# Optimization experiments

Hardware: AMD Instinct MI355X
Metric: run time of the kernel (lower is better)

The kernel has to match this reference:

```python
import jax, jax.numpy as jnp
import numpy as np

HEADS = 8
QK_DIM = 128
V_DIM = 128
QTD = 128   # query_token_dim
TTD = 128   # tgt_token_dim
B = 16384
H, W = 8, 6


def setup_inputs() -> dict:
    key = jax.random.key(0)
    ks = jax.random.split(key, 10)

    def lin(k, out_d, in_d):
        return jax.random.normal(k, (out_d, in_d), jnp.float32) * 0.02

    return {
        "query": jax.random.normal(ks[0], (1, 8, QTD), jnp.float32),
        "tgt_token": jax.random.normal(ks[1], (B, H * W, TTD), jnp.float32),
        "g1": jnp.ones((QTD,), jnp.float32),
        "b1": jnp.zeros((QTD,), jnp.float32),
        "Wq": lin(ks[2], QK_DIM, QTD), "bq": jnp.zeros((QK_DIM,), jnp.float32),
        "Wk": lin(ks[3], QK_DIM, TTD), "bk": jnp.zeros((QK_DIM,), jnp.float32),
        "Wv": lin(ks[4], V_DIM, TTD), "bv": jnp.zeros((V_DIM,), jnp.float32),
        "Wp": lin(ks[5], QTD, V_DIM), "bp": jnp.zeros((QTD,), jnp.float32),
        "g2": jnp.ones((QTD,), jnp.float32),
        "b2": jnp.zeros((QTD,), jnp.float32),
        "Wf1": lin(ks[6], QTD, QTD), "bf1": jnp.zeros((QTD,), jnp.float32),
        "Wf2": lin(ks[7], QTD, QTD), "bf2": jnp.zeros((QTD,), jnp.float32),
        "size_h": H,
        "size_w": W,
    }


def _ln(x, g, b, eps=1e-5):
    m = jnp.mean(x, axis=-1, keepdims=True)
    v = jnp.var(x, axis=-1, keepdims=True)
    return (x - m) * jax.lax.rsqrt(v + eps) * g + b


def _broad_mha(q, k, v):
    # BroadMultiHeadAttention: q [nq, Cq] broadcast over batch; k [Bk,M,Cq]; v [Bk,M,Cv]
    nq, Cq = q.shape
    Bk, M, Cv = v.shape
    d = Cq // HEADS
    qh = q.reshape(nq, HEADS, d).transpose(1, 0, 2)                   # [h, nq, d]
    kh = k.reshape(Bk, M, HEADS, d).transpose(0, 2, 1, 3)             # [b, h, M, d]
    vh = v.reshape(Bk, M, HEADS, Cv // HEADS).transpose(0, 2, 1, 3)   # [b, h, M, dv]
    dots = jnp.einsum('hid,bhjd->bhij', qh, kh) * (d ** -0.5)
    attn = jax.nn.softmax(dots, axis=-1)
    out = jnp.einsum('bhij,bhjd->bhid', attn, vh)                     # [b, h, nq, dv]
    return out.transpose(0, 2, 1, 3).reshape(Bk, nq, Cv)


def _forward(query, tgt_token, g1, b1, Wq, bq, Wk, bk, Wv, bv, Wp, bp,
             g2, b2, Wf1, bf1, Wf2, bf2, Hh, Ww):
    short_cut = query
    qn = _ln(query, g1, b1)
    q = qn @ Wq.T + bq            # [1, 8, qk_dim]
    k = tgt_token @ Wk.T + bk     # [B, HW, qk_dim]
    v = tgt_token @ Wv.T + bv     # [B, HW, v_dim]
    Bk = k.shape[0]
    q0 = q[0]                     # [8, qk_dim] (Q.squeeze() in the original)
    res = [_broad_mha(q0[:2], k, v)]
    k4 = k.reshape(Bk, Hh, Ww, QK_DIM)
    v4 = v.reshape(Bk, Hh, Ww, V_DIM)
    hs = [(0, Hh // 2), (Hh // 2, Hh)]
    ws = [(0, Ww // 3), (Ww // 3, 2 * (Ww // 3)), (2 * (Ww // 3), Ww)]
    idx = 0
    for h0, h1 in hs:
        for w0, w1 in ws:
            kw = k4[:, h0:h1, w0:w1].reshape(Bk, -1, QK_DIM)
            vw = v4[:, h0:h1, w0:w1].reshape(Bk, -1, V_DIM)
            res.append(_broad_mha(q0[2 + idx:3 + idx], kw, vw))
            idx += 1
    x = jnp.concatenate(res, axis=1)   # [B, 8, v_dim]
    x = short_cut + (x @ Wp.T + bp)    # broadcast residual: [1,8,D] + [B,8,D]
    y = _ln(x, g2, b2)
    y = jax.nn.gelu(y @ Wf1.T + bf1, approximate=False) @ Wf2.T + bf2
    return x + y


def reference(query, tgt_token, g1, b1, Wq, bq, Wk, bk, Wv, bv, Wp, bp,
              g2, b2, Wf1, bf1, Wf2, bf2, size_h, size_w):
    return _forward(query, tgt_token, g1, b1, Wq, bq, Wk, bk, Wv, bv, Wp, bp,
                    g2, b2, Wf1, bf1, Wf2, bf2, int(size_h), int(size_w))
```

## Files before the change

kernel.cpp:

```cpp
#include <hip/hip_runtime.h>
#include <math.h>


typedef __bf16 v8bf __attribute__((ext_vector_type(8)));
typedef float  v4f  __attribute__((ext_vector_type(4)));

static __device__ __forceinline__ v4f mfma16(v8bf a, v8bf b, v4f c) {
  return __builtin_amdgcn_mfma_f32_16x16x32_bf16(a, b, c, 0, 0, 0);
}

static __device__ __forceinline__ v8bf cvt8(const float* __restrict__ p) {
  float4 a = *(const float4*)p;
  float4 b = *(const float4*)(p + 4);
  v8bf f;
  f[0] = (__bf16)a.x; f[1] = (__bf16)a.y; f[2] = (__bf16)a.z; f[3] = (__bf16)a.w;
  f[4] = (__bf16)b.x; f[5] = (__bf16)b.y; f[6] = (__bf16)b.z; f[7] = (__bf16)b.w;
  return f;
}

__global__ __launch_bounds__(256)
void prep_kernel(const float* __restrict__ query,
                 const float* __restrict__ g1, const float* __restrict__ b1,
                 const float* __restrict__ Wq, const float* __restrict__ bq,
                 const float* __restrict__ Wk, const float* __restrict__ bk,
                 __bf16* __restrict__ qw, float* __restrict__ qb)
{
  __shared__ float qn[8*128];
  __shared__ float qp[8*128];
  const int t = threadIdx.x;
  for (int idx = t; idx < 1024; idx += 256) qn[idx] = query[idx];
  __syncthreads();
  {
    const int w = t >> 6, L = t & 63;
    const int row = 2*w + (L >> 5), col = L & 31;
    float x[4], s = 0.f, sq = 0.f;
    for (int p = 0; p < 4; p++) { x[p] = qn[row*128 + col + 32*p]; s += x[p]; sq += x[p]*x[p]; }
    for (int m = 1; m < 32; m <<= 1) { s += __shfl_xor(s, m); sq += __shfl_xor(sq, m); }
    const float mean = s * (1.f/128.f);
    const float var  = sq * (1.f/128.f) - mean*mean;
    const float rs   = rsqrtf(var + 1e-5f);
    for (int p = 0; p < 4; p++) {
      const int e = col + 32*p;
      qn[row*128 + e] = (x[p]-mean)*rs*g1[e] + b1[e];
    }
  }
  __syncthreads();
  {
    const int i = t >> 5, o0 = t & 31;
    for (int p = 0; p < 4; p++) {
      const int o = o0 + 32*p;
      float acc = bq[o];
      for (int e = 0; e < 128; e++) acc += qn[i*128 + e] * Wq[o*128 + e];
      qp[i*128 + o] = acc;
    }
  }
  __syncthreads();
  {
    const int cc = t >> 2, e0 = (t & 3) * 32;
    const int h = cc >> 3, i = cc & 7;
    float qv[16];
    for (int d = 0; d < 16; d++) qv[d] = qp[i*128 + 16*h + d];
    for (int e = e0; e < e0 + 32; e++) {
      float acc = 0.f;
      for (int d = 0; d < 16; d++) acc += qv[d] * Wk[(16*h + d)*128 + e];
      qw[cc*136 + e] = (__bf16)(0.25f * acc);
    }
    if (t < 64) {
      const int h2 = t >> 3, i2 = t & 7;
      float acc = 0.f;
      for (int d = 0; d < 16; d++) acc += qp[i2*128 + 16*h2 + d] * bk[16*h2 + d];
      qb[t] = 0.25f * acc;
    }
  }
}

__global__ __launch_bounds__(256)
void conv_kernel(const float* __restrict__ Wv, const float* __restrict__ Wp,
                 const float* __restrict__ Wf1, const float* __restrict__ Wf2,
                 __bf16* __restrict__ dst)
{
  const int m = blockIdx.x;
  const float* src = (m == 0) ? Wv : (m == 1) ? Wp : (m == 2) ? Wf1 : Wf2;
  __bf16* d = dst + m*16384;
  for (int i = threadIdx.x; i < 2048; i += 256)
    *(v8bf*)&d[i*8] = cvt8(&src[i*8]);
}

__global__ __launch_bounds__(256, 4)
void attn_kernel(const float* __restrict__ tgt,
                 const float* __restrict__ bv,
                 const __bf16* __restrict__ qw,
                 const float* __restrict__ qb,
                 const __bf16* __restrict__ wv,
                 float* __restrict__ xout)
{
  __shared__ __align__(16) __bf16 s_tgt[48*136];
  __shared__ __align__(16) __bf16 s_P[64*72];
  __shared__ __align__(16) __bf16 s_vT[128*72];

  const int b  = blockIdx.x;
  const int t  = threadIdx.x;
  const int w  = t >> 6;
  const int L  = t & 63;
  const int ln = L & 15;
  const int g  = L >> 4;

  for (int p = 0; p < 8; p++) {
    const int idx = 64*p + L;
    s_vT[(w*32 + (idx >> 4))*72 + 48 + (idx & 15)] = (__bf16)0.f;
  }
  for (int p = 0; p < 4; p++) {
    const int idx = 64*p + L;
    s_P[(w*16 + (idx >> 4))*72 + 48 + (idx & 15)] = (__bf16)0.f;
  }

  {
    const float* tg = tgt + (long)b * 6144;
    for (int c8 = t; c8 < 768; c8 += 256) {
      v8bf v = cvt8(&tg[c8*8]);
      *(v8bf*)&s_tgt[(c8 >> 4)*136 + (c8 & 15)*8] = v;
    }
  }
  __syncthreads();

  const int c = w*16 + ln;

  v4f dacc[3], vacc[3][2];
  {
    v8bf qwf[4], wvf[2][4];
    for (int ks = 0; ks < 4; ks++)
      qwf[ks] = *(const v8bf*)&qw[c*136 + ks*32 + g*8];
    for (int nt = 0; nt < 2; nt++)
      for (int ks = 0; ks < 4; ks++)
        wvf[nt][ks] = *(const v8bf*)&wv[(w*32 + nt*16 + ln)*128 + ks*32 + g*8];
    const v4f z = {0.f, 0.f, 0.f, 0.f};
    for (int mt = 0; mt < 3; mt++) { dacc[mt] = z; vacc[mt][0] = z; vacc[mt][1] = z; }
    for (int mt = 0; mt < 3; mt++) {
      v8bf af[4];
      for (int ks = 0; ks < 4; ks++)
        af[ks] = *(const v8bf*)&s_tgt[(mt*16 + ln)*136 + ks*32 + g*8];
      for (int ks = 0; ks < 4; ks++) {
        dacc[mt]    = mfma16(af[ks], qwf[ks],    dacc[mt]);
        vacc[mt][0] = mfma16(af[ks], wvf[0][ks], vacc[mt][0]);
        vacc[mt][1] = mfma16(af[ks], wvf[1][ks], vacc[mt][1]);
      }
    }
  }

  {
    const int i = c & 7;
    const float qbv = qb[c];
    const bool allv = (i < 2);
    int hsp = 0, wsp = 0;
    if (!allv) { const int idx = i - 2; hsp = idx / 3; wsp = idx - 3*hsp; }
    float dv[12];
    float mx = -1e30f;
    for (int mt = 0; mt < 3; mt++)
      for (int r = 0; r < 4; r++) {
        const int j  = mt*16 + g*4 + r;
        const int rr = j / 6, ccol = j - rr*6;
        const bool valid = allv || (((rr >> 2) == hsp) && ((ccol >> 1) == wsp));
        const float dd = valid ? dacc[mt][r] + qbv : -1e30f;
        dv[mt*4 + r] = dd;
        mx = fmaxf(mx, dd);
      }
    mx = fmaxf(mx, __shfl_xor(mx, 16));
    mx = fmaxf(mx, __shfl_xor(mx, 32));
    float sm = 0.f;
    for (int p = 0; p < 12; p++) {
      const float e = (dv[p] > -1e29f) ? __expf(dv[p] - mx) : 0.f;
      dv[p] = e; sm += e;
    }
    sm += __shfl_xor(sm, 16);
    sm += __shfl_xor(sm, 32);
    const float inv = 1.f / sm;
    for (int mt = 0; mt < 3; mt++)
      for (int r = 0; r < 4; r++)
        s_P[c*72 + mt*16 + g*4 + r] = (__bf16)(dv[mt*4 + r] * inv);
    for (int nt = 0; nt < 2; nt++) {
      const int o = w*32 + nt*16 + ln;
      const float bvo = bv[o];
      for (int mt = 0; mt < 3; mt++)
        for (int r = 0; r < 4; r++)
          s_vT[o*72 + mt*16 + g*4 + r] = (__bf16)(vacc[mt][nt][r] + bvo);
    }
  }

  {
    const v4f z = {0.f,0.f,0.f,0.f};
    v4f oacc[2] = {z, z};
    for (int ks = 0; ks < 2; ks++) {
      v8bf pf = *(const v8bf*)&s_P[(w*16 + ln)*72 + ks*32 + g*8];
      for (int nt = 0; nt < 2; nt++) {
        v8bf vf = *(const v8bf*)&s_vT[(w*32 + nt*16 + ln)*72 + ks*32 + g*8];
        oacc[nt] = mfma16(pf, vf, oacc[nt]);
      }
    }
    const int ntv = g >> 1;
    const int o = w*32 + ntv*16 + ln;
    float* xo = xout + (long)b * 1024;
    for (int r = 0; r < 4; r++) {
      const int i = (g*4 + r) & 7;
      xo[i*128 + o] = oacc[ntv][r];
    }
  }
}

__global__ __launch_bounds__(256, 4)
void mlp_kernel(const float* __restrict__ query,
                const float* __restrict__ bp,
                const float* __restrict__ g2, const float* __restrict__ b2,
                const float* __restrict__ bf1, const float* __restrict__ bf2,
                const __bf16* __restrict__ wp,
                const __bf16* __restrict__ wf1,
                const __bf16* __restrict__ wf2,
                float* __restrict__ xio)
{
  __shared__ __align__(16) __bf16 s_xn[4][16*136];
  __shared__ __align__(16) __bf16 s_h [4][16*136];

  const int t  = threadIdx.x;
  const int w  = t >> 6, L = t & 63;
  const int ln = L & 15, g = L >> 4;
  const long row0 = (long)blockIdx.x*64 + w*16;
  float* base = xio + row0*128;

  v8bf af[4];
  for (int ks = 0; ks < 4; ks++)
    af[ks] = cvt8(&base[ln*128 + ks*32 + g*8]);

  float x[8][4];
  for (int nt = 0; nt < 8; nt++) {
    v4f acc = {0.f, 0.f, 0.f, 0.f};
    for (int ks = 0; ks < 4; ks++) {
      v8bf wf = *(const v8bf*)&wp[(nt*16 + ln)*128 + ks*32 + g*8];
      acc = mfma16(af[ks], wf, acc);
    }
    const int col = nt*16 + ln;
    const float bpv = bp[col];
    for (int r = 0; r < 4; r++)
      x[nt][r] = acc[r] + bpv + query[((4*g + r) & 7)*128 + col];
  }

  float rmean[4], rrs[4];
  for (int r = 0; r < 4; r++) {
    float s = 0.f, sq = 0.f;
    for (int nt = 0; nt < 8; nt++) { s += x[nt][r]; sq += x[nt][r]*x[nt][r]; }
    for (int m = 1; m < 16; m <<= 1) { s += __shfl_xor(s, m); sq += __shfl_xor(sq, m); }
    const float mean = s * (1.f/128.f);
    const float var  = sq * (1.f/128.f) - mean*mean;
    rmean[r] = mean;
    rrs[r]   = rsqrtf(var + 1e-5f);
  }
  for (int nt = 0; nt < 8; nt++) {
    const int col = nt*16 + ln;
    const float gv = g2[col], b2v = b2[col];
    for (int r = 0; r < 4; r++)
      s_xn[w][(4*g + r)*136 + col] = (__bf16)((x[nt][r] - rmean[r])*rrs[r]*gv + b2v);
  }
  v8bf xf[4];
  for (int ks = 0; ks < 4; ks++)
    xf[ks] = *(const v8bf*)&s_xn[w][ln*136 + ks*32 + g*8];

  for (int nt = 0; nt < 8; nt++) {
    v4f acc = {0.f, 0.f, 0.f, 0.f};
    for (int ks = 0; ks < 4; ks++) {
      v8bf wf = *(const v8bf*)&wf1[(nt*16 + ln)*128 + ks*32 + g*8];
      acc = mfma16(xf[ks], wf, acc);
    }
    const int col = nt*16 + ln;
    const float b1v = bf1[col];
    for (int r = 0; r < 4; r++) {
      const float xx = acc[r] + b1v;
      s_h[w][(4*g + r)*136 + col] = (__bf16)(0.5f*xx*(1.f + erff(xx*0.70710678118654752f)));
    }
  }
  v8bf hf[4];
  for (int ks = 0; ks < 4; ks++)
    hf[ks] = *(const v8bf*)&s_h[w][ln*136 + ks*32 + g*8];

  for (int nt = 0; nt < 8; nt++) {
    v4f acc = {0.f, 0.f, 0.f, 0.f};
    for (int ks = 0; ks < 4; ks++) {
      v8bf wf = *(const v8bf*)&wf2[(nt*16 + ln)*128 + ks*32 + g*8];
      acc = mfma16(hf[ks], wf, acc);
    }
    const int col = nt*16 + ln;
    const float b2v = bf2[col];
    for (int r = 0; r < 4; r++)
      base[(4*g + r)*128 + col] = x[nt][r] + acc[r] + b2v;
  }
}

extern "C" void kernel_launch(void* const* d_in, const int* in_sizes, int n_in,
                              void* d_out, int out_size, void* d_ws, size_t ws_size,
                              hipStream_t stream)
{
  const float* query = (const float*)d_in[0];
  const float* tgt   = (const float*)d_in[1];
  const float* g1    = (const float*)d_in[2];
  const float* b1    = (const float*)d_in[3];
  const float* Wq    = (const float*)d_in[4];
  const float* bq    = (const float*)d_in[5];
  const float* Wk    = (const float*)d_in[6];
  const float* bk    = (const float*)d_in[7];
  const float* Wv    = (const float*)d_in[8];
  const float* bv    = (const float*)d_in[9];
  const float* Wp    = (const float*)d_in[10];
  const float* bp    = (const float*)d_in[11];
  const float* g2    = (const float*)d_in[12];
  const float* b2    = (const float*)d_in[13];
  const float* Wf1   = (const float*)d_in[14];
  const float* bf1   = (const float*)d_in[15];
  const float* Wf2   = (const float*)d_in[16];
  const float* bf2   = (const float*)d_in[17];
  float* out = (float*)d_out;

  __bf16* qw  = (__bf16*)d_ws;
  float*  qb  = (float*)((char*)d_ws + 64*136*2);
  __bf16* wbf = (__bf16*)((char*)d_ws + 64*136*2 + 256);

  const int nB = in_sizes[1] / (48 * 128);

  prep_kernel<<<1, 256, 0, stream>>>(query, g1, b1, Wq, bq, Wk, bk, qw, qb);
  conv_kernel<<<4, 256, 0, stream>>>(Wv, Wp, Wf1, Wf2, wbf);
  attn_kernel<<<nB, 256, 0, stream>>>(tgt, bv, qw, qb, wbf , out);
  mlp_kernel<<<nB/8, 256, 0, stream>>>(query, bp, g2, b2, bf1, bf2,
                                       wbf + 16384, wbf + 2*16384, wbf + 3*16384,
                                       out);
}
```

Before: 775.4 us.

## Fuse attention and MLP into one kernel with prefetched double-buffered tokens

Replaces the separate attention and MLP kernels with one kernel where each block handles 8 batch items. It keeps the attention output in shared memory as bf16 instead of writing it to global memory and reading it back. The next item's target tokens are prefetched into registers and staged through a double-buffered shared tile, and the two weight-prep kernels are merged into one launch. The cost is about 71 KB of shared memory per block and 8 serial iterations per block, which lowers occupancy and the number of blocks that can run at once.

```diff
diff --git a/kernel.cpp b/kernel.cpp
--- a/kernel.cpp
+++ b/kernel.cpp
@@ -18,16 +18,34 @@
   return f;
 }
 
+static __device__ __forceinline__ v8bf cvt2x4(float4 a, float4 b) {
+  v8bf f;
+  f[0] = (__bf16)a.x; f[1] = (__bf16)a.y; f[2] = (__bf16)a.z; f[3] = (__bf16)a.w;
+  f[4] = (__bf16)b.x; f[5] = (__bf16)b.y; f[6] = (__bf16)b.z; f[7] = (__bf16)b.w;
+  return f;
+}
+
 __global__ __launch_bounds__(256)
-void prep_kernel(const float* __restrict__ query,
-                 const float* __restrict__ g1, const float* __restrict__ b1,
-                 const float* __restrict__ Wq, const float* __restrict__ bq,
-                 const float* __restrict__ Wk, const float* __restrict__ bk,
-                 __bf16* __restrict__ qw, float* __restrict__ qb)
+void prep_conv_kernel(const float* __restrict__ query,
+                      const float* __restrict__ g1, const float* __restrict__ b1,
+                      const float* __restrict__ Wq, const float* __restrict__ bq,
+                      const float* __restrict__ Wk, const float* __restrict__ bk,
+                      const float* __restrict__ Wv, const float* __restrict__ Wp,
+                      const float* __restrict__ Wf1, const float* __restrict__ Wf2,
+                      __bf16* __restrict__ qw, float* __restrict__ qb,
+                      __bf16* __restrict__ wdst)
 {
   __shared__ float qn[8*128];
   __shared__ float qp[8*128];
   const int t = threadIdx.x;
+  const int m = blockIdx.x;
+  if (m < 4) {
+    const float* src = (m == 0) ? Wv : (m == 1) ? Wp : (m == 2) ? Wf1 : Wf2;
+    __bf16* d = wdst + m*16384;
+    for (int i = t; i < 2048; i += 256)
+      *(v8bf*)&d[i*8] = cvt8(&src[i*8]);
+    return;
+  }
   for (int idx = t; idx < 1024; idx += 256) qn[idx] = query[idx];
   __syncthreads();
   {
@@ -35,7 +53,7 @@
     const int row = 2*w + (L >> 5), col = L & 31;
     float x[4], s = 0.f, sq = 0.f;
     for (int p = 0; p < 4; p++) { x[p] = qn[row*128 + col + 32*p]; s += x[p]; sq += x[p]*x[p]; }
-    for (int m = 1; m < 32; m <<= 1) { s += __shfl_xor(s, m); sq += __shfl_xor(sq, m); }
+    for (int mm = 1; mm < 32; mm <<= 1) { s += __shfl_xor(s, mm); sq += __shfl_xor(sq, mm); }
     const float mean = s * (1.f/128.f);
     const float var  = sq * (1.f/128.f) - mean*mean;
     const float rs   = rsqrtf(var + 1e-5f);
@@ -74,36 +92,35 @@
   }
 }
 
-__global__ __launch_bounds__(256)
-void conv_kernel(const float* __restrict__ Wv, const float* __restrict__ Wp,
-                 const float* __restrict__ Wf1, const float* __restrict__ Wf2,
-                 __bf16* __restrict__ dst)
+__global__ __launch_bounds__(256, 4)
+void fused2_kernel(const float* __restrict__ tgt,
+                   const float* __restrict__ query,
+                   const float* __restrict__ qb,
+                   const float* __restrict__ bv,
+                   const float* __restrict__ bp,
+                   const float* __restrict__ g2, const float* __restrict__ b2,
+                   const float* __restrict__ bf1, const float* __restrict__ bf2,
+                   const __bf16* __restrict__ qw,
+                   const __bf16* __restrict__ wv,
+                   const __bf16* __restrict__ wp,
+                   const __bf16* __restrict__ wf1,
+                   const __bf16* __restrict__ wf2,
+                   float* __restrict__ out)
 {
-  const int m = blockIdx.x;
-  const float* src = (m == 0) ? Wv : (m == 1) ? Wp : (m == 2) ? Wf1 : Wf2;
-  __bf16* d = dst + m*16384;
-  for (int i = threadIdx.x; i < 2048; i += 256)
-    *(v8bf*)&d[i*8] = cvt8(&src[i*8]);
-}
-
-__global__ __launch_bounds__(256, 4)
-void attn_kernel(const float* __restrict__ tgt,
-                 const float* __restrict__ bv,
-                 const __bf16* __restrict__ qw,
-                 const float* __restrict__ qb,
-                 const __bf16* __restrict__ wv,
-                 float* __restrict__ xout)
-{
-  __shared__ __align__(16) __bf16 s_tgt[48*136];
-  __shared__ __align__(16) __bf16 s_P[64*72];
-  __shared__ __align__(16) __bf16 s_vT[128*72];
-
-  const int b  = blockIdx.x;
+  __shared__ __align__(16) char smem[71168];
+  __bf16* const s_tgt0 = (__bf16*)smem;
+  __bf16* const s_P    = (__bf16*)(smem + 26112);
+  __bf16* const s_vT   = (__bf16*)(smem + 35328);
+  __bf16* const s_act  = (__bf16*)(smem + 53760);
+  __bf16* const s_h    = (__bf16*)smem;
+  __bf16* const s_xn   = (__bf16*)(smem + 35328);
+
   const int t  = threadIdx.x;
   const int w  = t >> 6;
   const int L  = t & 63;
   const int ln = L & 15;
   const int g  = L >> 4;
+  const long b0 = (long)blockIdx.x * 8;
 
   for (int p = 0; p < 8; p++) {
     const int idx = 64*p + L;
@@ -114,120 +131,123 @@
     s_P[(w*16 + (idx >> 4))*72 + 48 + (idx & 15)] = (__bf16)0.f;
   }
 
+  const int c = w*16 + ln;
+  const float qbv = qb[c];
+  const int qi = c & 7;
+  const bool allv = (qi < 2);
+  int hsp = 0, wsp = 0;
+  if (!allv) { const int idx = qi - 2; hsp = idx / 3; wsp = idx - 3*hsp; }
+
+  float4 pf[6];
   {
-    const float* tg = tgt + (long)b * 6144;
-    for (int c8 = t; c8 < 768; c8 += 256) {
-      v8bf v = cvt8(&tg[c8*8]);
-      *(v8bf*)&s_tgt[(c8 >> 4)*136 + (c8 & 15)*8] = v;
-    }
-  }
-  __syncthreads();
-
-  const int c = w*16 + ln;
-
-  v4f dacc[3], vacc[3][2];
-  {
-    v8bf qwf[4], wvf[2][4];
-    for (int ks = 0; ks < 4; ks++)
-      qwf[ks] = *(const v8bf*)&qw[c*136 + ks*32 + g*8];
-    for (int nt = 0; nt < 2; nt++)
+    const float* tg = tgt + b0 * 6144;
+#pragma unroll
+    for (int k2 = 0; k2 < 3; k2++) {
+      pf[2*k2]   = *(const float4*)&tg[(t + k2*256)*8];
+      pf[2*k2+1] = *(const float4*)&tg[(t + k2*256)*8 + 4];
+    }
+  }
+
+  for (int bi = 0; bi < 8; bi++) {
+    __bf16* const s_tgt = s_tgt0 + (bi & 1) * 6528;
+
+#pragma unroll
+    for (int k2 = 0; k2 < 3; k2++) {
+      const int c8 = t + k2*256;
+      *(v8bf*)&s_tgt[(c8 >> 4)*136 + (c8 & 15)*8] = cvt2x4(pf[2*k2], pf[2*k2+1]);
+    }
+    __syncthreads();
+
+    if (bi < 7) {
+      const float* tg = tgt + (b0 + bi + 1) * 6144;
+#pragma unroll
+      for (int k2 = 0; k2 < 3; k2++) {
+        pf[2*k2]   = *(const float4*)&tg[(t + k2*256)*8];
+        pf[2*k2+1] = *(const float4*)&tg[(t + k2*256)*8 + 4];
+      }
+    }
+
+    v4f dacc[3], vacc[3][2];
+    {
+      v8bf qwf[4], wvf[2][4];
       for (int ks = 0; ks < 4; ks++)
-        wvf[nt][ks] = *(const v8bf*)&wv[(w*32 + nt*16 + ln)*128 + ks*32 + g*8];
-    const v4f z = {0.f, 0.f, 0.f, 0.f};
-    for (int mt = 0; mt < 3; mt++) { dacc[mt] = z; vacc[mt][0] = z; vacc[mt][1] = z; }
-    for (int mt = 0; mt < 3; mt++) {
-      v8bf af[4];
-      for (int ks = 0; ks < 4; ks++)
-        af[ks] = *(const v8bf*)&s_tgt[(mt*16 + ln)*136 + ks*32 + g*8];
-      for (int ks = 0; ks < 4; ks++) {
-        dacc[mt]    = mfma16(af[ks], qwf[ks],    dacc[mt]);
-        vacc[mt][0] = mfma16(af[ks], wvf[0][ks], vacc[mt][0]);
-        vacc[mt][1] = mfma16(af[ks], wvf[1][ks], vacc[mt][1]);
-      }
-    }
-  }
-
-  {
-    const int i = c & 7;
-    const float qbv = qb[c];
-    const bool allv = (i < 2);
-    int hsp = 0, wsp = 0;
-    if (!allv) { const int idx = i - 2; hsp = idx / 3; wsp = idx - 3*hsp; }
-    float dv[12];
-    float mx = -1e30f;
-    for (int mt = 0; mt < 3; mt++)
-      for (int r = 0; r < 4; r++) {
-        const int j  = mt*16 + g*4 + r;
-        const int rr = j / 6, ccol = j - rr*6;
-        const bool valid = allv || (((rr >> 2) == hsp) && ((ccol >> 1) == wsp));
-        const float dd = valid ? dacc[mt][r] + qbv : -1e30f;
-        dv[mt*4 + r] = dd;
-        mx = fmaxf(mx, dd);
-      }
-    mx = fmaxf(mx, __shfl_xor(mx, 16));
-    mx = fmaxf(mx, __shfl_xor(mx, 32));
-    float sm = 0.f;
-    for (int p = 0; p < 12; p++) {
-      const float e = (dv[p] > -1e29f) ? __expf(dv[p] - mx) : 0.f;
-      dv[p] = e; sm += e;
-    }
-    sm += __shfl_xor(sm, 16);
-    sm += __shfl_xor(sm, 32);
-    const float inv = 1.f / sm;
-    for (int mt = 0; mt < 3; mt++)
-      for (int r = 0; r < 4; r++)
-        s_P[c*72 + mt*16 + g*4 + r] = (__bf16)(dv[mt*4 + r] * inv);
-    for (int nt = 0; nt < 2; nt++) {
-      const int o = w*32 + nt*16 + ln;
-      const float bvo = bv[o];
+        qwf[ks] = *(const v8bf*)&qw[c*136 + ks*32 + g*8];
+      for (int nt = 0; nt < 2; nt++)
+        for (int ks = 0; ks < 4; ks++)
+          wvf[nt][ks] = *(const v8bf*)&wv[(w*32 + nt*16 + ln)*128 + ks*32 + g*8];
+      const v4f z = {0.f, 0.f, 0.f, 0.f};
+      for (int mt = 0; mt < 3; mt++) { dacc[mt] = z; vacc[mt][0] = z; vacc[mt][1] = z; }
+      for (int mt = 0; mt < 3; mt++) {
+        v8bf af[4];
+        for (int ks = 0; ks < 4; ks++)
+          af[ks] = *(const v8bf*)&s_tgt[(mt*16 + ln)*136 + ks*32 + g*8];
+        for (int ks = 0; ks < 4; ks++) {
+          dacc[mt]    = mfma16(af[ks], qwf[ks],    dacc[mt]);
+          vacc[mt][0] = mfma16(af[ks], wvf[0][ks], vacc[mt][0]);
+          vacc[mt][1] = mfma16(af[ks], wvf[1][ks], vacc[mt][1]);
+        }
+      }
+    }
+
+    {
+      float dv[12];
+      float mx = -1e30f;
+      for (int mt = 0; mt < 3; mt++)
+        for (int r = 0; r < 4; r++) {
+          const int j  = mt*16 + g*4 + r;
+          const int rr = j / 6, ccol = j - rr*6;
+          const bool valid = allv || (((rr >> 2) == hsp) && ((ccol >> 1) == wsp));
+          const float dd = valid ? dacc[mt][r] + qbv : -1e30f;
+          dv[mt*4 + r] = dd;
+          mx = fmaxf(mx, dd);
+        }
+      mx = fmaxf(mx, __shfl_xor(mx, 16));
+      mx = fmaxf(mx, __shfl_xor(mx, 32));
+      float sm = 0.f;
+      for (int p = 0; p < 12; p++) {
+        const float e = (dv[p] > -1e29f) ? __expf(dv[p] - mx) : 0.f;
+        dv[p] = e; sm += e;
+      }
+      sm += __shfl_xor(sm, 16);
+      sm += __shfl_xor(sm, 32);
+      const float inv = 1.f / sm;
       for (int mt = 0; mt < 3; mt++)
         for (int r = 0; r < 4; r++)
-          s_vT[o*72 + mt*16 + g*4 + r] = (__bf16)(vacc[mt][nt][r] + bvo);
-    }
-  }
-
-  {
-    const v4f z = {0.f,0.f,0.f,0.f};
-    v4f oacc[2] = {z, z};
-    for (int ks = 0; ks < 2; ks++) {
-      v8bf pf = *(const v8bf*)&s_P[(w*16 + ln)*72 + ks*32 + g*8];
+          s_P[c*72 + mt*16 + g*4 + r] = (__bf16)(dv[mt*4 + r] * inv);
       for (int nt = 0; nt < 2; nt++) {
-        v8bf vf = *(const v8bf*)&s_vT[(w*32 + nt*16 + ln)*72 + ks*32 + g*8];
-        oacc[nt] = mfma16(pf, vf, oacc[nt]);
-      }
-    }
-    const int ntv = g >> 1;
-    const int o = w*32 + ntv*16 + ln;
-    float* xo = xout + (long)b * 1024;
-    for (int r = 0; r < 4; r++) {
-      const int i = (g*4 + r) & 7;
-      xo[i*128 + o] = oacc[ntv][r];
-    }
-  }
-}
-
-__global__ __launch_bounds__(256, 4)
-void mlp_kernel(const float* __restrict__ query,
-                const float* __restrict__ bp,
-                const float* __restrict__ g2, const float* __restrict__ b2,
-                const float* __restrict__ bf1, const float* __restrict__ bf2,
-                const __bf16* __restrict__ wp,
-                const __bf16* __restrict__ wf1,
-                const __bf16* __restrict__ wf2,
-                float* __restrict__ xio)
-{
-  __shared__ __align__(16) __bf16 s_xn[4][16*136];
-  __shared__ __align__(16) __bf16 s_h [4][16*136];
-
-  const int t  = threadIdx.x;
-  const int w  = t >> 6, L = t & 63;
-  const int ln = L & 15, g = L >> 4;
-  const long row0 = (long)blockIdx.x*64 + w*16;
-  float* base = xio + row0*128;
+        const int o = w*32 + nt*16 + ln;
+        const float bvo = bv[o];
+        for (int mt = 0; mt < 3; mt++)
+          for (int r = 0; r < 4; r++)
+            s_vT[o*72 + mt*16 + g*4 + r] = (__bf16)(vacc[mt][nt][r] + bvo);
+      }
+    }
+
+    {
+      const v4f z = {0.f,0.f,0.f,0.f};
+      v4f oacc[2] = {z, z};
+      for (int ks = 0; ks < 2; ks++) {
+        v8bf pfrag = *(const v8bf*)&s_P[(w*16 + ln)*72 + ks*32 + g*8];
+        for (int nt = 0; nt < 2; nt++) {
+          v8bf vf = *(const v8bf*)&s_vT[(w*32 + nt*16 + ln)*72 + ks*32 + g*8];
+          oacc[nt] = mfma16(pfrag, vf, oacc[nt]);
+        }
+      }
+      const int ntv = g >> 1;
+      const int o = w*32 + ntv*16 + ln;
+      for (int r = 0; r < 4; r++) {
+        const int i = (g*4 + r) & 7;
+        s_act[(bi*8 + i)*136 + o] = (__bf16)oacc[ntv][r];
+      }
+    }
+  }
+  __syncthreads();
+
+  float* base = out + ((long)blockIdx.x*64 + w*16)*128;
 
   v8bf af[4];
   for (int ks = 0; ks < 4; ks++)
-    af[ks] = cvt8(&base[ln*128 + ks*32 + g*8]);
+    af[ks] = *(const v8bf*)&s_act[(w*16 + ln)*136 + ks*32 + g*8];
 
   float x[8][4];
   for (int nt = 0; nt < 8; nt++) {
@@ -246,7 +266,7 @@
   for (int r = 0; r < 4; r++) {
     float s = 0.f, sq = 0.f;
     for (int nt = 0; nt < 8; nt++) { s += x[nt][r]; sq += x[nt][r]*x[nt][r]; }
-    for (int m = 1; m < 16; m <<= 1) { s += __shfl_xor(s, m); sq += __shfl_xor(sq, m); }
+    for (int mm = 1; mm < 16; mm <<= 1) { s += __shfl_xor(s, mm); sq += __shfl_xor(sq, mm); }
     const float mean = s * (1.f/128.f);
     const float var  = sq * (1.f/128.f) - mean*mean;
     rmean[r] = mean;
@@ -256,11 +276,11 @@
     const int col = nt*16 + ln;
     const float gv = g2[col], b2v = b2[col];
     for (int r = 0; r < 4; r++)
-      s_xn[w][(4*g + r)*136 + col] = (__bf16)((x[nt][r] - rmean[r])*rrs[r]*gv + b2v);
+      s_xn[w*2176 + (4*g + r)*136 + col] = (__bf16)((x[nt][r] - rmean[r])*rrs[r]*gv + b2v);
   }
   v8bf xf[4];
   for (int ks = 0; ks < 4; ks++)
-    xf[ks] = *(const v8bf*)&s_xn[w][ln*136 + ks*32 + g*8];
+    xf[ks] = *(const v8bf*)&s_xn[w*2176 + ln*136 + ks*32 + g*8];
 
   for (int nt = 0; nt < 8; nt++) {
     v4f acc = {0.f, 0.f, 0.f, 0.f};
@@ -272,12 +292,12 @@
     const float b1v = bf1[col];
     for (int r = 0; r < 4; r++) {
       const float xx = acc[r] + b1v;
-      s_h[w][(4*g + r)*136 + col] = (__bf16)(0.5f*xx*(1.f + erff(xx*0.70710678118654752f)));
+      s_h[w*2176 + (4*g + r)*136 + col] = (__bf16)(0.5f*xx*(1.f + erff(xx*0.70710678118654752f)));
     }
   }
   v8bf hf[4];
   for (int ks = 0; ks < 4; ks++)
-    hf[ks] = *(const v8bf*)&s_h[w][ln*136 + ks*32 + g*8];
+    hf[ks] = *(const v8bf*)&s_h[w*2176 + ln*136 + ks*32 + g*8];
 
   for (int nt = 0; nt < 8; nt++) {
     v4f acc = {0.f, 0.f, 0.f, 0.f};
@@ -322,10 +342,10 @@
 
   const int nB = in_sizes[1] / (48 * 128);
 
-  prep_kernel<<<1, 256, 0, stream>>>(query, g1, b1, Wq, bq, Wk, bk, qw, qb);
-  conv_kernel<<<4, 256, 0, stream>>>(Wv, Wp, Wf1, Wf2, wbf);
-  attn_kernel<<<nB, 256, 0, stream>>>(tgt, bv, qw, qb, wbf , out);
-  mlp_kernel<<<nB/8, 256, 0, stream>>>(query, bp, g2, b2, bf1, bf2,
-                                       wbf + 16384, wbf + 2*16384, wbf + 3*16384,
-                                       out);
-}
+  prep_conv_kernel<<<5, 256, 0, stream>>>(query, g1, b1, Wq, bq, Wk, bk,
+                                          Wv, Wp, Wf1, Wf2, qw, qb, wbf);
+  fused2_kernel<<<nB/8, 256, 0, stream>>>(tgt, query, qb, bv, bp, g2, b2,
+                                          bf1, bf2, qw,
+                                          wbf, wbf + 16384, wbf + 2*16384, wbf + 3*16384,
+                                          out);
+}
```

Result: faster. 709.6 us (-8.5%).
